# Optimization experiments

Measured on AMD Instinct MI355X. Metric: run time of the kernel, lower is better.

## Reference

```python
import jax, jax.numpy as jnp
import numpy as np

N = 4096
F_IN = 256
HEADS = 8
FEAT = 64
NEG_SLOPE = 0.2


def setup_inputs() -> dict:
    key = jax.random.key(0)
    k_x, k_adj, k_w, k_s, k_d = jax.random.split(key, 5)
    x = jax.random.normal(k_x, (N, F_IN), dtype=jnp.float32)
    adj = (jax.random.uniform(k_adj, (N, N)) < 0.02).astype(jnp.float32)
    W = jax.random.normal(k_w, (F_IN, HEADS * FEAT), dtype=jnp.float32) * (1.0 / np.sqrt(F_IN))
    a_src = jax.random.normal(k_s, (FEAT,), dtype=jnp.float32) * (1.0 / np.sqrt(FEAT))
    a_dst = jax.random.normal(k_d, (FEAT,), dtype=jnp.float32) * (1.0 / np.sqrt(FEAT))
    return {"x": x, "adj": adj, "W": W, "a_src": a_src, "a_dst": a_dst}


def reference(x, adj, W, a_src, a_dst):
    n = x.shape[0]
    adj = adj + jnp.eye(n, dtype=adj.dtype)          # add self loops
    h = (x @ W).reshape(n, HEADS, FEAT)              # (N, H, F)
    s_src = jnp.einsum('nhf,f->nh', h, a_src)        # (N, H)
    s_dst = jnp.einsum('nhf,f->nh', h, a_dst)        # (N, H)
    # e[i, j, h] = leaky_relu(s_src[i,h] + s_dst[j,h])  -> (N, N, H)
    e = jax.nn.leaky_relu(s_src[:, None, :] + s_dst[None, :, :], negative_slope=NEG_SLOPE)
    mask = (adj == 0)                                # (N, N)
    e = jnp.where(mask[:, :, None], -1e9, e)
    alpha = jax.nn.softmax(e, axis=1)                # softmax over neighbor axis j
    out = jnp.einsum('ijh,jhf->ihf', alpha, h)       # (N, H, F)
    return out.reshape(n, HEADS * FEAT)              # concat heads -> (N, 512)
```

## Files before the change

### kernel.cpp

```cpp
#include <hip/hip_runtime.h>
#include <hip/hip_fp16.h>
#include <stdint.h>

#define NROWS 4096
#define FIN   256
#define NHEADS 8
#define HF    512
#define NEG   0.2f
#define MAXDEG 144

typedef _Float16 half8_t  __attribute__((ext_vector_type(8)));
typedef float    float4_t __attribute__((ext_vector_type(4)));

__global__ __launch_bounds__(256) void k_prep(const float* __restrict__ x,
                                              const float* __restrict__ W,
                                              _Float16* __restrict__ xh,
                                              _Float16* __restrict__ Wt) {
    const int bid = blockIdx.x, t = threadIdx.x;
    if (bid < 1024) {
        const int i4 = (bid*256 + t) * 4;
        float4 v = *(const float4*)&x[i4];
        union { _Float16 h[4]; uint2 u; } P;
        P.h[0] = (_Float16)v.x; P.h[1] = (_Float16)v.y;
        P.h[2] = (_Float16)v.z; P.h[3] = (_Float16)v.w;
        *(uint2*)&xh[i4] = P.u;
    } else {
        const int i4 = ((bid - 1024)*256 + t) * 4;
        const int n = i4 >> 8, k0 = i4 & 255;
        union { _Float16 h[4]; uint2 u; } P;
        P.h[0] = (_Float16)W[(size_t)(k0+0)*HF + n];
        P.h[1] = (_Float16)W[(size_t)(k0+1)*HF + n];
        P.h[2] = (_Float16)W[(size_t)(k0+2)*HF + n];
        P.h[3] = (_Float16)W[(size_t)(k0+3)*HF + n];
        *(uint2*)&Wt[(size_t)n*FIN + k0] = P.u;
    }
}

__global__ __launch_bounds__(256) void k_gemm(const _Float16* __restrict__ xh,
                                              const _Float16* __restrict__ Wt,
                                              const float* __restrict__ a_src,
                                              const float* __restrict__ a_dst,
                                              _Float16* __restrict__ hfp,
                                              float* __restrict__ s_src,
                                              float* __restrict__ s_dst) {
    __shared__ _Float16 Ah[64][72];
    __shared__ _Float16 Bh[64][72];
    const int t = threadIdx.x;
    const int bm = blockIdx.x >> 3, bn = blockIdx.x & 7;
    const int lane = t & 63, w = t >> 6;
    const int wm = (w & 1) * 32, wn = (w >> 1) * 32;
    const int mrow = lane & 15, kch = (lane >> 4) * 8;
    const int sr = t >> 2, sc = (t & 3) << 4;

    float4_t acc00{}, acc01{}, acc10{}, acc11{};

    for (int kt = 0; kt < FIN; kt += 64) {
        uint4 a0 = *(const uint4*)&xh[(size_t)(bm*64 + sr)*FIN + kt + sc];
        uint4 a1 = *(const uint4*)&xh[(size_t)(bm*64 + sr)*FIN + kt + sc + 8];
        uint4 b0 = *(const uint4*)&Wt[(size_t)(bn*64 + sr)*FIN + kt + sc];
        uint4 b1 = *(const uint4*)&Wt[(size_t)(bn*64 + sr)*FIN + kt + sc + 8];
        __syncthreads();
        *(uint4*)&Ah[sr][sc]     = a0;  *(uint4*)&Ah[sr][sc + 8] = a1;
        *(uint4*)&Bh[sr][sc]     = b0;  *(uint4*)&Bh[sr][sc + 8] = b1;
        __syncthreads();
        #pragma unroll
        for (int kk = 0; kk < 64; kk += 32) {
            half8_t fa0 = *(const half8_t*)&Ah[wm + mrow][kk + kch];
            half8_t fa1 = *(const half8_t*)&Ah[wm + 16 + mrow][kk + kch];
            half8_t fb0 = *(const half8_t*)&Bh[wn + mrow][kk + kch];
            half8_t fb1 = *(const half8_t*)&Bh[wn + 16 + mrow][kk + kch];
            acc00 = __builtin_amdgcn_mfma_f32_16x16x32_f16(fa0, fb0, acc00, 0, 0, 0);
            acc01 = __builtin_amdgcn_mfma_f32_16x16x32_f16(fa0, fb1, acc01, 0, 0, 0);
            acc10 = __builtin_amdgcn_mfma_f32_16x16x32_f16(fa1, fb0, acc10, 0, 0, 0);
            acc11 = __builtin_amdgcn_mfma_f32_16x16x32_f16(fa1, fb1, acc11, 0, 0, 0);
        }
    }

    __syncthreads();
    const int crow = (lane >> 4) * 4;
    #pragma unroll
    for (int r = 0; r < 4; ++r) {
        Ah[wm + crow + r][wn + mrow]           = (_Float16)acc00[r];
        Ah[wm + crow + r][wn + 16 + mrow]      = (_Float16)acc01[r];
        Ah[wm + 16 + crow + r][wn + mrow]      = (_Float16)acc10[r];
        Ah[wm + 16 + crow + r][wn + 16 + mrow] = (_Float16)acc11[r];
    }
    __syncthreads();

    uint4 h0 = *(const uint4*)&Ah[sr][sc];
    uint4 h1 = *(const uint4*)&Ah[sr][sc + 8];
    *(uint4*)&hfp[(size_t)(bm*64 + sr)*HF + bn*64 + sc]     = h0;
    *(uint4*)&hfp[(size_t)(bm*64 + sr)*HF + bn*64 + sc + 8] = h1;

    union { uint4 u[2]; _Float16 h[16]; } H; H.u[0] = h0; H.u[1] = h1;
    float ps = 0.f, pd = 0.f;
    #pragma unroll
    for (int e = 0; e < 16; ++e) {
        float hv = (float)H.h[e];
        ps += hv * a_src[sc + e];
        pd += hv * a_dst[sc + e];
    }
    ps += __shfl_xor(ps, 1); ps += __shfl_xor(ps, 2);
    pd += __shfl_xor(pd, 1); pd += __shfl_xor(pd, 2);
    if ((t & 3) == 0) {
        s_src[(bm*64 + sr)*NHEADS + bn] = ps;
        s_dst[(bm*64 + sr)*NHEADS + bn] = pd;
    }
}

__global__ __launch_bounds__(256) void k_agg(const float* __restrict__ adj,
                                             const float* __restrict__ s_src,
                                             const float* __restrict__ s_dst,
                                             const _Float16* __restrict__ hfp,
                                             float* __restrict__ out) {
    __shared__ float    abuf[4][MAXDEG][8];
    __shared__ uint32_t nbrs[4][MAXDEG];
    __shared__ float    hsum[4][8];

    const int t = threadIdx.x, w = t >> 6, lane = t & 63;
    const int row = blockIdx.x * 4 + w;

    const float* ar = adj + (size_t)row * NROWS + lane*4;
    float4 f[16];
    #pragma unroll
    for (int k = 0; k < 16; ++k) f[k] = *(const float4*)(ar + k*256);

    uint64_t pm = 0;
    #pragma unroll
    for (int k = 0; k < 16; ++k) {
        if (f[k].x != 0.f) pm |= 1ull << (k*4+0);
        if (f[k].y != 0.f) pm |= 1ull << (k*4+1);
        if (f[k].z != 0.f) pm |= 1ull << (k*4+2);
        if (f[k].w != 0.f) pm |= 1ull << (k*4+3);
    }
    if (((row >> 2) & 63) == lane)
        pm |= 1ull << (((row >> 8) << 2) | (row & 3));

    int pcnt = __popcll(pm);
    int incl = pcnt;
    #pragma unroll
    for (int d = 1; d < 64; d <<= 1) {
        int u = __shfl_up(incl, d);
        if (lane >= d) incl += u;
    }
    int cnt = __shfl(incl, 63);
    int pos = incl - pcnt;
    if (cnt > MAXDEG) cnt = MAXDEG;
    const int pad8 = (cnt + 7) & ~7;

    uint64_t m = pm;
    while (m) {
        int q = (int)__ffsll((unsigned long long)m);  q -= 1;  m &= m - 1;
        int col = ((q >> 2) << 8) + lane*4 + (q & 3);
        if (pos < MAXDEG) nbrs[w][pos] = (uint32_t)col << 10;
        pos++;
    }
    for (int p = cnt + lane; p < pad8; p += 64) nbrs[w][p] = 0;
    __builtin_amdgcn_wave_barrier();

    float4 si0 = *(const float4*)&s_src[row*NHEADS];
    float4 si1 = *(const float4*)&s_src[row*NHEADS + 4];
    float ac0=0,ac1=0,ac2=0,ac3=0,ac4=0,ac5=0,ac6=0,ac7=0;
    #pragma unroll 1
    for (int base = 0; base < pad8; base += 64) {
        int p = base + lane;
        if (p < pad8) {
            float a0=0,a1=0,a2=0,a3=0,a4=0,a5=0,a6=0,a7=0;
            if (p < cnt) {
                int j8 = (int)(nbrs[w][p] >> 10) * NHEADS;
                float4 d0 = *(const float4*)&s_dst[j8];
                float4 d1 = *(const float4*)&s_dst[j8 + 4];
                float e;
                e = si0.x + d0.x; e = e > 0.f ? e : NEG*e; a0 = __expf(e);
                e = si0.y + d0.y; e = e > 0.f ? e : NEG*e; a1 = __expf(e);
                e = si0.z + d0.z; e = e > 0.f ? e : NEG*e; a2 = __expf(e);
                e = si0.w + d0.w; e = e > 0.f ? e : NEG*e; a3 = __expf(e);
                e = si1.x + d1.x; e = e > 0.f ? e : NEG*e; a4 = __expf(e);
                e = si1.y + d1.y; e = e > 0.f ? e : NEG*e; a5 = __expf(e);
                e = si1.z + d1.z; e = e > 0.f ? e : NEG*e; a6 = __expf(e);
                e = si1.w + d1.w; e = e > 0.f ? e : NEG*e; a7 = __expf(e);
            }
            abuf[w][p][0]=a0; abuf[w][p][1]=a1; abuf[w][p][2]=a2; abuf[w][p][3]=a3;
            abuf[w][p][4]=a4; abuf[w][p][5]=a5; abuf[w][p][6]=a6; abuf[w][p][7]=a7;
            ac0+=a0; ac1+=a1; ac2+=a2; ac3+=a3; ac4+=a4; ac5+=a5; ac6+=a6; ac7+=a7;
        }
    }
    #pragma unroll
    for (int msk = 1; msk < 64; msk <<= 1) {
        ac0 += __shfl_xor(ac0, msk); ac1 += __shfl_xor(ac1, msk);
        ac2 += __shfl_xor(ac2, msk); ac3 += __shfl_xor(ac3, msk);
        ac4 += __shfl_xor(ac4, msk); ac5 += __shfl_xor(ac5, msk);
        ac6 += __shfl_xor(ac6, msk); ac7 += __shfl_xor(ac7, msk);
    }
    if (lane == 0) {
        hsum[w][0]=ac0; hsum[w][1]=ac1; hsum[w][2]=ac2; hsum[w][3]=ac3;
        hsum[w][4]=ac4; hsum[w][5]=ac5; hsum[w][6]=ac6; hsum[w][7]=ac7;
    }
    __builtin_amdgcn_wave_barrier();

    const int h3 = lane >> 3;
    const float invg = 1.f / hsum[w][h3];
    const uint32_t n0 = nbrs[w][lane];
    const uint32_t n1 = nbrs[w][64 + lane];
    const char* hbase = (const char*)hfp;
    float c0=0,c1=0,c2=0,c3=0,c4=0,c5=0,c6=0,c7=0;

#define GBATCH(JOEXPR)                                                      \
    {                                                                       \
        uint32_t jo[8]; uint4 hv[8]; float aa[8];                           \
        _Pragma("unroll") for (int u = 0; u < 8; ++u) jo[u] = (JOEXPR);     \
        _Pragma("unroll") for (int u = 0; u < 8; ++u)                       \
            hv[u] = *(const uint4*)(hbase + jo[u] + lane*16);               \
        _Pragma("unroll") for (int u = 0; u < 8; ++u)                       \
            aa[u] = abuf[w][p + u][h3];                                     \
        _Pragma("unroll") for (int u = 0; u < 8; ++u) {                     \
            union { uint4 q; _Float16 h[8]; } U; U.q = hv[u];               \
            c0 += (float)U.h[0]*aa[u]; c1 += (float)U.h[1]*aa[u];           \
            c2 += (float)U.h[2]*aa[u]; c3 += (float)U.h[3]*aa[u];           \
            c4 += (float)U.h[4]*aa[u]; c5 += (float)U.h[5]*aa[u];           \
            c6 += (float)U.h[6]*aa[u]; c7 += (float)U.h[7]*aa[u];           \
        }                                                                   \
    }

    const int e1 = pad8 < 64 ? pad8 : 64;
    for (int p = 0; p < e1; p += 8) GBATCH(__shfl(n0, p + u))
    if (pad8 > 64) {
        const int e2 = pad8 < 128 ? pad8 : 128;
        for (int p = 64; p < e2; p += 8) GBATCH(__shfl(n1, p + u - 64))
        for (int p = 128; p < pad8; p += 8) GBATCH(nbrs[w][p + u])
    }
#undef GBATCH

    float* orow = out + (size_t)row*HF + lane*8;
    *(float4*)(orow)     = make_float4(c0*invg, c1*invg, c2*invg, c3*invg);
    *(float4*)(orow + 4) = make_float4(c4*invg, c5*invg, c6*invg, c7*invg);
}

extern "C" void kernel_launch(void* const* d_in, const int* in_sizes, int n_in,
                              void* d_out, int out_size, void* d_ws, size_t ws_size,
                              hipStream_t stream) {
    const float* x     = (const float*)d_in[0];
    const float* adj   = (const float*)d_in[1];
    const float* W     = (const float*)d_in[2];
    const float* a_src = (const float*)d_in[3];
    const float* a_dst = (const float*)d_in[4];
    float* out = (float*)d_out;

    char* ws = (char*)d_ws;
    _Float16* hfp   = (_Float16*)ws;
    float*    s_src = (float*)(ws + 4u*1024*1024);
    float*    s_dst = (float*)(ws + 4u*1024*1024 + 128u*1024);
    _Float16* xh    = (_Float16*)(ws + 4u*1024*1024 + 256u*1024);
    _Float16* Wt    = (_Float16*)(ws + 6u*1024*1024 + 256u*1024);

    k_prep<<<1152, 256, 0, stream>>>(x, W, xh, Wt);
    k_gemm<<<512,  256, 0, stream>>>(xh, Wt, a_src, a_dst, hfp, s_src, s_dst);
    k_agg <<<1024, 256, 0, stream>>>(adj, s_src, s_dst, hfp, out);
}
```

Measured before the change: 45.13 us.

## Process two rows per wave in aggregation, prefetching both adjacency rows upfront

The aggregation kernel now gives each wave two rows (row and row+2048) and launches half as many blocks. Both 16 KB adjacency rows are loaded into registers before either is processed, so the second row's load overlaps the first row's compute. LDS attention-weight stores are also vectorised to float4. This holds 128 floats of adjacency in registers per thread, with launch bounds asking for 2 blocks per CU, which risks register pressure or spilling and fewer waves in flight.

```diff
diff --git a/kernel.cpp b/kernel.cpp
--- a/kernel.cpp
+++ b/kernel.cpp
@@ -108,23 +108,13 @@
     }
 }
 
-__global__ __launch_bounds__(256) void k_agg(const float* __restrict__ adj,
-                                             const float* __restrict__ s_src,
-                                             const float* __restrict__ s_dst,
-                                             const _Float16* __restrict__ hfp,
-                                             float* __restrict__ out) {
-    __shared__ float    abuf[4][MAXDEG][8];
-    __shared__ uint32_t nbrs[4][MAXDEG];
-    __shared__ float    hsum[4][8];
-
-    const int t = threadIdx.x, w = t >> 6, lane = t & 63;
-    const int row = blockIdx.x * 4 + w;
-
-    const float* ar = adj + (size_t)row * NROWS + lane*4;
-    float4 f[16];
-    #pragma unroll
-    for (int k = 0; k < 16; ++k) f[k] = *(const float4*)(ar + k*256);
-
+__device__ __forceinline__ void row_phase(int row, int w, int lane,
+    const float4* f,
+    const float* __restrict__ s_src, const float* __restrict__ s_dst,
+    const _Float16* __restrict__ hfp, float* __restrict__ out,
+    float (*__restrict__ abuf)[8], uint32_t* __restrict__ nbrs,
+    float* __restrict__ hsum)
+{
     uint64_t pm = 0;
     #pragma unroll
     for (int k = 0; k < 16; ++k) {
@@ -152,10 +142,10 @@
     while (m) {
         int q = (int)__ffsll((unsigned long long)m);  q -= 1;  m &= m - 1;
         int col = ((q >> 2) << 8) + lane*4 + (q & 3);
-        if (pos < MAXDEG) nbrs[w][pos] = (uint32_t)col << 10;
+        if (pos < MAXDEG) nbrs[pos] = (uint32_t)col << 10;
         pos++;
     }
-    for (int p = cnt + lane; p < pad8; p += 64) nbrs[w][p] = 0;
+    for (int p = cnt + lane; p < pad8; p += 64) nbrs[p] = 0;
     __builtin_amdgcn_wave_barrier();
 
     float4 si0 = *(const float4*)&s_src[row*NHEADS];
@@ -167,7 +157,7 @@
         if (p < pad8) {
             float a0=0,a1=0,a2=0,a3=0,a4=0,a5=0,a6=0,a7=0;
             if (p < cnt) {
-                int j8 = (int)(nbrs[w][p] >> 10) * NHEADS;
+                int j8 = (int)(nbrs[p] >> 10) * NHEADS;
                 float4 d0 = *(const float4*)&s_dst[j8];
                 float4 d1 = *(const float4*)&s_dst[j8 + 4];
                 float e;
@@ -180,8 +170,8 @@
                 e = si1.z + d1.z; e = e > 0.f ? e : NEG*e; a6 = __expf(e);
                 e = si1.w + d1.w; e = e > 0.f ? e : NEG*e; a7 = __expf(e);
             }
-            abuf[w][p][0]=a0; abuf[w][p][1]=a1; abuf[w][p][2]=a2; abuf[w][p][3]=a3;
-            abuf[w][p][4]=a4; abuf[w][p][5]=a5; abuf[w][p][6]=a6; abuf[w][p][7]=a7;
+            *(float4*)&abuf[p][0] = make_float4(a0, a1, a2, a3);
+            *(float4*)&abuf[p][4] = make_float4(a4, a5, a6, a7);
             ac0+=a0; ac1+=a1; ac2+=a2; ac3+=a3; ac4+=a4; ac5+=a5; ac6+=a6; ac7+=a7;
         }
     }
@@ -193,15 +183,15 @@
         ac6 += __shfl_xor(ac6, msk); ac7 += __shfl_xor(ac7, msk);
     }
     if (lane == 0) {
-        hsum[w][0]=ac0; hsum[w][1]=ac1; hsum[w][2]=ac2; hsum[w][3]=ac3;
-        hsum[w][4]=ac4; hsum[w][5]=ac5; hsum[w][6]=ac6; hsum[w][7]=ac7;
+        hsum[0]=ac0; hsum[1]=ac1; hsum[2]=ac2; hsum[3]=ac3;
+        hsum[4]=ac4; hsum[5]=ac5; hsum[6]=ac6; hsum[7]=ac7;
     }
     __builtin_amdgcn_wave_barrier();
 
     const int h3 = lane >> 3;
-    const float invg = 1.f / hsum[w][h3];
-    const uint32_t n0 = nbrs[w][lane];
-    const uint32_t n1 = nbrs[w][64 + lane];
+    const float invg = 1.f / hsum[h3];
+    const uint32_t n0 = nbrs[lane];
+    const uint32_t n1 = nbrs[64 + lane];
     const char* hbase = (const char*)hfp;
     float c0=0,c1=0,c2=0,c3=0,c4=0,c5=0,c6=0,c7=0;
 
@@ -212,7 +202,7 @@
         _Pragma("unroll") for (int u = 0; u < 8; ++u)                       \
             hv[u] = *(const uint4*)(hbase + jo[u] + lane*16);               \
         _Pragma("unroll") for (int u = 0; u < 8; ++u)                       \
-            aa[u] = abuf[w][p + u][h3];                                     \
+            aa[u] = abuf[p + u][h3];                                        \
         _Pragma("unroll") for (int u = 0; u < 8; ++u) {                     \
             union { uint4 q; _Float16 h[8]; } U; U.q = hv[u];               \
             c0 += (float)U.h[0]*aa[u]; c1 += (float)U.h[1]*aa[u];           \
@@ -227,13 +217,41 @@
     if (pad8 > 64) {
         const int e2 = pad8 < 128 ? pad8 : 128;
         for (int p = 64; p < e2; p += 8) GBATCH(__shfl(n1, p + u - 64))
-        for (int p = 128; p < pad8; p += 8) GBATCH(nbrs[w][p + u])
+        for (int p = 128; p < pad8; p += 8) GBATCH(nbrs[p + u])
     }
 #undef GBATCH
 
     float* orow = out + (size_t)row*HF + lane*8;
     *(float4*)(orow)     = make_float4(c0*invg, c1*invg, c2*invg, c3*invg);
     *(float4*)(orow + 4) = make_float4(c4*invg, c5*invg, c6*invg, c7*invg);
+    __builtin_amdgcn_wave_barrier();
+}
+
+__global__ __launch_bounds__(256, 2) void k_agg(const float* __restrict__ adj,
+                                                const float* __restrict__ s_src,
+                                                const float* __restrict__ s_dst,
+                                                const _Float16* __restrict__ hfp,
+                                                float* __restrict__ out) {
+    __shared__ float    ABUF[4][MAXDEG][8];
+    __shared__ uint32_t NBRS[4][MAXDEG];
+    __shared__ float    HSUM[4][8];
+
+    const int t = threadIdx.x, w = t >> 6, lane = t & 63;
+    const int wid = blockIdx.x * 4 + w;
+    const int rA = wid, rB = wid + 2048;
+
+    float4 fA[16], fB[16];
+    {
+        const float* arA = adj + (size_t)rA * NROWS + lane*4;
+        const float* arB = adj + (size_t)rB * NROWS + lane*4;
+        #pragma unroll
+        for (int k = 0; k < 16; ++k) fA[k] = *(const float4*)(arA + k*256);
+        #pragma unroll
+        for (int k = 0; k < 16; ++k) fB[k] = *(const float4*)(arB + k*256);
+    }
+
+    row_phase(rA, w, lane, fA, s_src, s_dst, hfp, out, ABUF[w], NBRS[w], HSUM[w]);
+    row_phase(rB, w, lane, fB, s_src, s_dst, hfp, out, ABUF[w], NBRS[w], HSUM[w]);
 }
 
 extern "C" void kernel_launch(void* const* d_in, const int* in_sizes, int n_in,
@@ -255,5 +273,5 @@
 
     k_prep<<<1152, 256, 0, stream>>>(x, W, xh, Wt);
     k_gemm<<<512,  256, 0, stream>>>(xh, Wt, a_src, a_dst, hfp, s_src, s_dst);
-    k_agg <<<1024, 256, 0, stream>>>(adj, s_src, s_dst, hfp, out);
-}
+    k_agg <<<512,  256, 0, stream>>>(adj, s_src, s_dst, hfp, out);
+}
```

Result: slower. 53.23 us (+17.9%).

## Move adjacency scan into prep kernel and pass compact neighbor lists to aggregation

Applied to the files above, without the earlier changes.

The dense adjacency scan and neighbor-list compaction move out of the aggregation kernel into the first staging kernel, which runs alongside the x/W fp16 conversion. They write 16-bit neighbor indices and degrees to workspace, and the aggregation kernel then reads only these compact lists. The 64 MB adjacency read now sits in the first kernel, where its blocks run concurrently with the conversion work, which is meant to shorten the aggregation critical path. The change adds a global round trip for the neighbor lists and also vectorises the LDS stores of attention weights.

```diff
diff --git a/kernel.cpp b/kernel.cpp
--- a/kernel.cpp
+++ b/kernel.cpp
@@ -12,20 +12,74 @@
 typedef _Float16 half8_t  __attribute__((ext_vector_type(8)));
 typedef float    float4_t __attribute__((ext_vector_type(4)));
 
-__global__ __launch_bounds__(256) void k_prep(const float* __restrict__ x,
-                                              const float* __restrict__ W,
-                                              _Float16* __restrict__ xh,
-                                              _Float16* __restrict__ Wt) {
+__global__ __launch_bounds__(256) void k_stage(const float* __restrict__ adj,
+                                               const float* __restrict__ x,
+                                               const float* __restrict__ W,
+                                               uint16_t* __restrict__ nbr_g,
+                                               int* __restrict__ deg,
+                                               _Float16* __restrict__ xh,
+                                               _Float16* __restrict__ Wt) {
+    __shared__ uint16_t cnbr[4][MAXDEG];
     const int bid = blockIdx.x, t = threadIdx.x;
+
     if (bid < 1024) {
-        const int i4 = (bid*256 + t) * 4;
+        const int w = t >> 6, lane = t & 63;
+        const int row = bid*4 + w;
+
+        uint32_t* nb32 = (uint32_t*)cnbr[w];
+        nb32[lane] = 0;
+        if (lane < (MAXDEG/2 - 64)) nb32[64 + lane] = 0;
+        __builtin_amdgcn_wave_barrier();
+
+        const float* ar = adj + (size_t)row * NROWS + lane*4;
+        float4 f[16];
+        #pragma unroll
+        for (int k = 0; k < 16; ++k) f[k] = *(const float4*)(ar + k*256);
+
+        uint64_t pm = 0;
+        #pragma unroll
+        for (int k = 0; k < 16; ++k) {
+            if (f[k].x != 0.f) pm |= 1ull << (k*4+0);
+            if (f[k].y != 0.f) pm |= 1ull << (k*4+1);
+            if (f[k].z != 0.f) pm |= 1ull << (k*4+2);
+            if (f[k].w != 0.f) pm |= 1ull << (k*4+3);
+        }
+        if (((row >> 2) & 63) == lane)
+            pm |= 1ull << (((row >> 8) << 2) | (row & 3));
+
+        int pcnt = __popcll(pm);
+        int incl = pcnt;
+        #pragma unroll
+        for (int d = 1; d < 64; d <<= 1) {
+            int u = __shfl_up(incl, d);
+            if (lane >= d) incl += u;
+        }
+        int cnt = __shfl(incl, 63);
+        int pos = incl - pcnt;
+        if (cnt > MAXDEG) cnt = MAXDEG;
+
+        uint64_t m = pm;
+        while (m) {
+            int q = (int)__ffsll((unsigned long long)m) - 1;  m &= m - 1;
+            int col = ((q >> 2) << 8) + lane*4 + (q & 3);
+            if (pos < MAXDEG) cnbr[w][pos] = (uint16_t)col;
+            pos++;
+        }
+        __builtin_amdgcn_wave_barrier();
+
+        uint32_t* og = (uint32_t*)(nbr_g + (size_t)row * MAXDEG);
+        og[lane] = nb32[lane];
+        if (lane < (MAXDEG/2 - 64)) og[64 + lane] = nb32[64 + lane];
+        if (lane == 0) deg[row] = cnt;
+    } else if (bid < 2048) {
+        const int i4 = ((bid - 1024)*256 + t) * 4;
         float4 v = *(const float4*)&x[i4];
         union { _Float16 h[4]; uint2 u; } P;
         P.h[0] = (_Float16)v.x; P.h[1] = (_Float16)v.y;
         P.h[2] = (_Float16)v.z; P.h[3] = (_Float16)v.w;
         *(uint2*)&xh[i4] = P.u;
     } else {
-        const int i4 = ((bid - 1024)*256 + t) * 4;
+        const int i4 = ((bid - 2048)*256 + t) * 4;
         const int n = i4 >> 8, k0 = i4 & 255;
         union { _Float16 h[4]; uint2 u; } P;
         P.h[0] = (_Float16)W[(size_t)(k0+0)*HF + n];
@@ -108,7 +162,8 @@
     }
 }
 
-__global__ __launch_bounds__(256) void k_agg(const float* __restrict__ adj,
+__global__ __launch_bounds__(256) void k_agg(const uint16_t* __restrict__ nbr_g,
+                                             const int* __restrict__ deg,
                                              const float* __restrict__ s_src,
                                              const float* __restrict__ s_dst,
                                              const _Float16* __restrict__ hfp,
@@ -120,42 +175,19 @@
     const int t = threadIdx.x, w = t >> 6, lane = t & 63;
     const int row = blockIdx.x * 4 + w;
 
-    const float* ar = adj + (size_t)row * NROWS + lane*4;
-    float4 f[16];
-    #pragma unroll
-    for (int k = 0; k < 16; ++k) f[k] = *(const float4*)(ar + k*256);
-
-    uint64_t pm = 0;
-    #pragma unroll
-    for (int k = 0; k < 16; ++k) {
-        if (f[k].x != 0.f) pm |= 1ull << (k*4+0);
-        if (f[k].y != 0.f) pm |= 1ull << (k*4+1);
-        if (f[k].z != 0.f) pm |= 1ull << (k*4+2);
-        if (f[k].w != 0.f) pm |= 1ull << (k*4+3);
-    }
-    if (((row >> 2) & 63) == lane)
-        pm |= 1ull << (((row >> 8) << 2) | (row & 3));
-
-    int pcnt = __popcll(pm);
-    int incl = pcnt;
-    #pragma unroll
-    for (int d = 1; d < 64; d <<= 1) {
-        int u = __shfl_up(incl, d);
-        if (lane >= d) incl += u;
-    }
-    int cnt = __shfl(incl, 63);
-    int pos = incl - pcnt;
+    int cnt = deg[row];
     if (cnt > MAXDEG) cnt = MAXDEG;
     const int pad8 = (cnt + 7) & ~7;
 
-    uint64_t m = pm;
-    while (m) {
-        int q = (int)__ffsll((unsigned long long)m);  q -= 1;  m &= m - 1;
-        int col = ((q >> 2) << 8) + lane*4 + (q & 3);
-        if (pos < MAXDEG) nbrs[w][pos] = (uint32_t)col << 10;
-        pos++;
-    }
-    for (int p = cnt + lane; p < pad8; p += 64) nbrs[w][p] = 0;
+    const uint32_t* src32 = (const uint32_t*)(nbr_g + (size_t)row * MAXDEG);
+    uint32_t v0 = src32[lane];
+    nbrs[w][2*lane]     = (v0 & 0xffffu) << 10;
+    nbrs[w][2*lane + 1] = (v0 >> 16) << 10;
+    if (lane < (MAXDEG/2 - 64)) {
+        uint32_t v1 = src32[64 + lane];
+        nbrs[w][128 + 2*lane] = (v1 & 0xffffu) << 10;
+        nbrs[w][129 + 2*lane] = (v1 >> 16) << 10;
+    }
     __builtin_amdgcn_wave_barrier();
 
     float4 si0 = *(const float4*)&s_src[row*NHEADS];
@@ -180,8 +212,8 @@
                 e = si1.z + d1.z; e = e > 0.f ? e : NEG*e; a6 = __expf(e);
                 e = si1.w + d1.w; e = e > 0.f ? e : NEG*e; a7 = __expf(e);
             }
-            abuf[w][p][0]=a0; abuf[w][p][1]=a1; abuf[w][p][2]=a2; abuf[w][p][3]=a3;
-            abuf[w][p][4]=a4; abuf[w][p][5]=a5; abuf[w][p][6]=a6; abuf[w][p][7]=a7;
+            *(float4*)&abuf[w][p][0] = make_float4(a0, a1, a2, a3);
+            *(float4*)&abuf[w][p][4] = make_float4(a4, a5, a6, a7);
             ac0+=a0; ac1+=a1; ac2+=a2; ac3+=a3; ac4+=a4; ac5+=a5; ac6+=a6; ac7+=a7;
         }
     }
@@ -252,8 +284,10 @@
     float*    s_dst = (float*)(ws + 4u*1024*1024 + 128u*1024);
     _Float16* xh    = (_Float16*)(ws + 4u*1024*1024 + 256u*1024);
     _Float16* Wt    = (_Float16*)(ws + 6u*1024*1024 + 256u*1024);
-
-    k_prep<<<1152, 256, 0, stream>>>(x, W, xh, Wt);
-    k_gemm<<<512,  256, 0, stream>>>(xh, Wt, a_src, a_dst, hfp, s_src, s_dst);
-    k_agg <<<1024, 256, 0, stream>>>(adj, s_src, s_dst, hfp, out);
-}
+    uint16_t* nbr_g = (uint16_t*)(ws + 6u*1024*1024 + 512u*1024);
+    int*      deg   = (int*)(ws + 7u*1024*1024 + 768u*1024);
+
+    k_stage<<<2176, 256, 0, stream>>>(adj, x, W, nbr_g, deg, xh, Wt);
+    k_gemm <<<512,  256, 0, stream>>>(xh, Wt, a_src, a_dst, hfp, s_src, s_dst);
+    k_agg  <<<1024, 256, 0, stream>>>(nbr_g, deg, s_src, s_dst, hfp, out);
+}
```

Result: slower. 47.88 us (+6.1%).
